# Performance work log

Measured on AMD Instinct MI355X. Metric: run time of the kernel, lower is better.

## Reference

```python
import jax, jax.numpy as jnp
import numpy as np

B, N, D, H = 128, 128, 1024, 8
HD = D // H  # 128; NOTE: N must equal HD due to the module's einsum pattern
SCALE = HD ** -0.5


def _split_heads(x):
    # [b, n, h*d] -> [b, h, n, d]
    b, n, _ = x.shape
    return x.reshape(b, n, H, HD).transpose(0, 2, 1, 3)


def setup_inputs() -> dict:
    key = jax.random.key(0)
    ks = jax.random.split(key, 12)
    s = D ** -0.5
    return {
        "words": jax.random.normal(ks[0], (B, N, D), jnp.float32),
        "position": jax.random.normal(ks[1], (B, N, D), jnp.float32),
        "conscious": jax.random.normal(ks[2], (B, N, D), jnp.float32),
        "Wq_w": jax.random.normal(ks[3], (D, D), jnp.float32) * s,
        "Wk_w": jax.random.normal(ks[4], (D, D), jnp.float32) * s,
        "Wv_w": jax.random.normal(ks[5], (D, D), jnp.float32) * s,
        "Wq_p": jax.random.normal(ks[6], (D, D), jnp.float32) * s,
        "Wk_p": jax.random.normal(ks[7], (D, D), jnp.float32) * s,
        "Wq_c": jax.random.normal(ks[8], (D, D), jnp.float32) * s,
        "Wk_c": jax.random.normal(ks[9], (D, D), jnp.float32) * s,
        "Wo": jax.random.normal(ks[10], (D, D), jnp.float32) * s,
        "bo": jax.random.normal(ks[11], (D,), jnp.float32) * 0.01,
    }


def reference(words, position, conscious, Wq_w, Wk_w, Wv_w, Wq_p, Wk_p, Wq_c, Wk_c, Wo, bo):
    q_w = _split_heads(words @ Wq_w)
    k_w = _split_heads(words @ Wk_w)
    v_w = _split_heads(words @ Wv_w)
    q_p = _split_heads(position @ Wq_p)
    k_p = _split_heads(position @ Wk_p)
    q_c = _split_heads(conscious @ Wq_c)
    k_c = _split_heads(conscious @ Wk_c)

    # Faithful to source: 'b h i j, b h j d -> b h i d' contracts q's head dim
    # with k's seq dim (requires N == HD). Three score streams summed.
    sim = (jnp.einsum('bhij,bhjd->bhid', q_w, k_w)
           + jnp.einsum('bhij,bhjd->bhid', q_p, k_p)
           + jnp.einsum('bhij,bhjd->bhid', q_c, k_c)) * SCALE
    attn = jax.nn.softmax(sim, axis=-1)
    out = jnp.einsum('bhij,bhjd->bhid', attn, v_w)  # [b,h,n,d]
    out = out.transpose(0, 2, 1, 3).reshape(B, N, D)  # merge heads
    return out @ Wo + bo
```

## Files before the change

### kernel.cpp

```cpp
#include <hip/hip_runtime.h>


typedef unsigned short u16;
typedef __attribute__((ext_vector_type(8))) short bf16x8;
typedef __attribute__((ext_vector_type(4))) short bf16x4;
typedef __attribute__((ext_vector_type(4))) float f32x4;

__device__ __forceinline__ float bf2f(u16 x) {
  union { unsigned u; float f; } v;
  v.u = ((unsigned)x) << 16;
  return v.f;
}

__device__ __forceinline__ u16 f2bf(float f) {
  union { float f; unsigned u; } v;
  v.f = f;
  unsigned r = v.u + 0x7fffu + ((v.u >> 16) & 1u);
  return (u16)(r >> 16);
}

__device__ __forceinline__ float ldv(const void* p, size_t i, int f32) {
  return f32 ? ((const float*)p)[i] : bf2f(((const u16*)p)[i]);
}

__device__ __forceinline__ f32x4 MFMA(bf16x8 a, bf16x8 b, f32x4 c) {
  return __builtin_amdgcn_mfma_f32_16x16x32_bf16(a, b, c, 0, 0, 0);
}

#define GLDS16(gp, lp)                                               \
  __builtin_amdgcn_global_load_lds(                                  \
      (const __attribute__((address_space(1))) unsigned int*)(gp),   \
      (__attribute__((address_space(3))) unsigned int*)(lp), 16, 0, 0)

__device__ __forceinline__ bf16x8 lds_frag(const u16* ls, int row, int cb) {
  const int byte = (row * 128 + cb) ^ ((row & 7) << 4);
  return *(const bf16x8*)((const char*)ls + byte);
}

__device__ __forceinline__ int cs_byte(int row, int colb) {
  return (row * 256 + colb) ^ ((row & 7) << 4);
}

__global__ void detect_dtype(const void* words, int* flag) {
  __shared__ int cnt;
  if (threadIdx.x == 0) cnt = 0;
  __syncthreads();
  const u16* w = (const u16*)words;
  int local = 0;
  for (int i = threadIdx.x; i < 2048; i += 256) {
    const u16 v = w[2 * i];
    const int e = (v >> 7) & 0xFF;
    if (v == 0 || (e >= 0x60 && e <= 0x8F)) local++;
  }
  atomicAdd(&cnt, local);
  __syncthreads();
  if (threadIdx.x == 0) *flag = (cnt >= 1434) ? 0 : 1;
}

__global__ __launch_bounds__(256) void cast_w(
    const void* w0, const void* w1, const void* w2, const void* w3,
    const void* w4, const void* w5, const void* w6, const void* w7,
    u16* __restrict__ WT, const int* __restrict__ flag) {
  __shared__ float t[32][33];
  const int f32 = *flag;
  const int p = blockIdx.z;
  const void* W;
  switch (p) {
    case 0: W = w0; break; case 1: W = w1; break; case 2: W = w2; break;
    case 3: W = w3; break; case 4: W = w4; break; case 5: W = w5; break;
    case 6: W = w6; break; default: W = w7; break;
  }
  const int k0 = blockIdx.y * 32, n0 = blockIdx.x * 32;
  const int tx = threadIdx.x & 31, ry = threadIdx.x >> 5;
  for (int r = ry; r < 32; r += 8)
    t[r][tx] = ldv(W, (size_t)(k0 + r) * 1024 + n0 + tx, f32);
  __syncthreads();
  u16* dst = WT + (size_t)p * 1048576ull;
  for (int r = ry; r < 32; r += 8)
    dst[(size_t)(n0 + r) * 1024 + k0 + tx] = f2bf(t[tx][r]);
}

__global__ __launch_bounds__(256) void cast_a(
    const void* x0, const void* x1, const void* x2, u16* __restrict__ Abf,
    int b0, int chb, const int* __restrict__ flag) {
  const int f32 = *flag;
  const int t = blockIdx.z;
  const void* src = (t == 0) ? x0 : ((t == 1) ? x1 : x2);
  u16* dst = Abf + (size_t)t * (size_t)chb * 131072ull;
  const size_t n4 = (size_t)chb * 32768ull;
  const size_t off = (size_t)b0 * 131072ull;
  const size_t stride = (size_t)gridDim.x * 256ull;
  if (f32) {
    const float4* s = (const float4*)src + off / 4;
    for (size_t i = (size_t)blockIdx.x * 256 + threadIdx.x; i < n4; i += stride) {
      const float4 v = s[i];
      bf16x4 o = { (short)f2bf(v.x), (short)f2bf(v.y),
                   (short)f2bf(v.z), (short)f2bf(v.w) };
      *(bf16x4*)&dst[i * 4] = o;
    }
  } else {
    const bf16x4* s = (const bf16x4*)((const u16*)src + off);
    for (size_t i = (size_t)blockIdx.x * 256 + threadIdx.x; i < n4; i += stride)
      ((bf16x4*)dst)[i] = s[i];
  }
}

__global__ __launch_bounds__(256) void proj_mfma(
    const u16* __restrict__ Abf, const u16* __restrict__ WT,
    u16* __restrict__ P, int chb) {
  __shared__ u16 lds[16384];
  u16* lsA = lds;
  u16* lsB = lds + 8192;
  const int p = blockIdx.z;
  const int asel = (p < 3) ? 0 : ((p < 5) ? 1 : 2);
  const u16* A = Abf + (size_t)asel * (size_t)chb * 131072ull;
  const u16* W = WT + (size_t)p * 1048576ull;
  u16* C = P + (size_t)p * (size_t)chb * 131072ull;
  const int tr = (p == 1) | (p == 2) | (p == 4) | (p == 6);

  int wg = blockIdx.y * 8 + blockIdx.x;
  const int nwg = (int)gridDim.y * 8;
  wg = (wg & 7) * (nwg >> 3) + (wg >> 3);
  const int bx = wg & 7, by = wg >> 3;

  const int tn = bx * 128;
  const int tm = by * 128;
  const int w = threadIdx.x >> 6, l = threadIdx.x & 63;
  const int wm = w >> 1, wn = w & 1;
  const int lr = l >> 3;
  const int lc = ((l & 7) * 16) ^ (lr << 4);
  const int fr = l & 15, fq = l >> 4;

  f32x4 acc[4][4] = {};
  for (int kt = 0; kt < 1024; kt += 64) {
    #pragma unroll
    for (int c = 0; c < 4; ++c) {
      GLDS16(&A[(size_t)(tm + w * 32 + c * 8 + lr) * 1024 + kt + (lc >> 1)],
             &lsA[(w * 32 + c * 8) * 64]);
      GLDS16(&W[(size_t)(tn + w * 32 + c * 8 + lr) * 1024 + kt + (lc >> 1)],
             &lsB[(w * 32 + c * 8) * 64]);
    }
    __syncthreads();
    #pragma unroll
    for (int ks = 0; ks < 2; ++ks) {
      bf16x8 af[4], bfr[4];
      const int cb = ks * 64 + fq * 16;
      #pragma unroll
      for (int m = 0; m < 4; ++m)
        af[m] = lds_frag(lsA, wm * 64 + m * 16 + fr, cb);
      #pragma unroll
      for (int n = 0; n < 4; ++n)
        bfr[n] = lds_frag(lsB, wn * 64 + n * 16 + fr, cb);
      #pragma unroll
      for (int m = 0; m < 4; ++m)
        #pragma unroll
        for (int n = 0; n < 4; ++n)
          acc[m][n] = MFMA(af[m], bfr[n], acc[m][n]);
    }
    __syncthreads();
  }

  #pragma unroll
  for (int m = 0; m < 4; ++m)
    #pragma unroll
    for (int n = 0; n < 4; ++n)
      #pragma unroll
      for (int r = 0; r < 4; ++r) {
        const int row = wm * 64 + m * 16 + fq * 4 + r;
        const int col = wn * 64 + n * 16 + fr;
        const int sr = tr ? col : row;
        const int sc = tr ? row : col;
        *(u16*)((char*)lds + cs_byte(sr, sc * 2)) = f2bf(acc[m][n][r]);
      }
  __syncthreads();
  const int crow = threadIdx.x >> 4;
  const int ccb = (threadIdx.x & 15) * 16;
  if (!tr) {
    #pragma unroll
    for (int pass = 0; pass < 8; ++pass) {
      const int row = pass * 16 + crow;
      const bf16x8 v = *(const bf16x8*)((const char*)lds + cs_byte(row, ccb));
      *(bf16x8*)&C[(size_t)(tm + row) * 1024 + tn + (ccb >> 1)] = v;
    }
  } else {
    const size_t tb = ((size_t)by * 8 + bx) * 16384ull;
    #pragma unroll
    for (int pass = 0; pass < 8; ++pass) {
      const int d = pass * 16 + crow;
      const bf16x8 v = *(const bf16x8*)((const char*)lds + cs_byte(d, ccb));
      *(bf16x8*)&C[tb + (size_t)d * 128 + (ccb >> 1)] = v;
    }
  }
}

__global__ __launch_bounds__(256) void attn_mfma(
    const u16* __restrict__ P, int chb, u16* __restrict__ merged) {
  __shared__ u16 pl[16384];
  const int h = blockIdx.x, b = blockIdx.y;
  const int w = threadIdx.x >> 6, l = threadIdx.x & 63;
  const size_t MS = (size_t)chb * 131072ull;
  const u16* const Qs[3] = { P, P + 3 * MS, P + 5 * MS };
  const u16* const Ks[3] = { P + 1 * MS, P + 4 * MS, P + 6 * MS };
  const u16* V = P + 2 * MS;
  const size_t qb = (size_t)b * 131072ull + (size_t)h * 128;
  const size_t kb = ((size_t)b * 8 + h) * 16384ull;

  f32x4 acc[2][8] = {};
  #pragma unroll
  for (int kt = 0; kt < 128; kt += 32) {
    #pragma unroll
    for (int t = 0; t < 3; ++t) {
      bf16x8 a[2];
      #pragma unroll
      for (int m = 0; m < 2; ++m)
        a[m] = *(const bf16x8*)&Qs[t][qb + (size_t)(w * 32 + m * 16 + (l & 15)) * 1024
                                       + kt + (l >> 4) * 8];
      #pragma unroll
      for (int n = 0; n < 8; ++n) {
        const bf16x8 bb = *(const bf16x8*)&Ks[t][kb + (size_t)(n * 16 + (l & 15)) * 128
                                                 + kt + (l >> 4) * 8];
        acc[0][n] = MFMA(a[0], bb, acc[0][n]);
        acc[1][n] = MFMA(a[1], bb, acc[1][n]);
      }
    }
  }

  const float SC = 0.08838834764831845f;
  #pragma unroll
  for (int m = 0; m < 2; ++m)
    #pragma unroll
    for (int r = 0; r < 4; ++r) {
      float mx = -3.0e38f;
      #pragma unroll
      for (int n = 0; n < 8; ++n) {
        acc[m][n][r] *= SC;
        mx = fmaxf(mx, acc[m][n][r]);
      }
      #pragma unroll
      for (int s = 1; s < 16; s <<= 1) mx = fmaxf(mx, __shfl_xor(mx, s));
      float sm = 0.f;
      #pragma unroll
      for (int n = 0; n < 8; ++n) {
        const float e = __expf(acc[m][n][r] - mx);
        acc[m][n][r] = e;
        sm += e;
      }
      #pragma unroll
      for (int s = 1; s < 16; s <<= 1) sm += __shfl_xor(sm, s);
      const float inv = 1.f / sm;
      #pragma unroll
      for (int n = 0; n < 8; ++n) acc[m][n][r] *= inv;
    }

  #pragma unroll
  for (int m = 0; m < 2; ++m)
    #pragma unroll
    for (int n = 0; n < 8; ++n)
      #pragma unroll
      for (int r = 0; r < 4; ++r) {
        const int row = w * 32 + m * 16 + (l >> 4) * 4 + r;
        const int col = n * 16 + (l & 15);
        const int byte = (row * 256 + col * 2) ^ ((row & 7) << 4);
        *(u16*)((char*)pl + byte) = f2bf(acc[m][n][r]);
      }
  __syncthreads();

  f32x4 o[2][8] = {};
  #pragma unroll
  for (int kt = 0; kt < 128; kt += 32) {
    bf16x8 a[2];
    #pragma unroll
    for (int m = 0; m < 2; ++m) {
      const int row = w * 32 + m * 16 + (l & 15);
      const int byte = (row * 256 + (kt + (l >> 4) * 8) * 2) ^ ((row & 7) << 4);
      a[m] = *(const bf16x8*)((char*)pl + byte);
    }
    #pragma unroll
    for (int n = 0; n < 8; ++n) {
      const bf16x8 bb = *(const bf16x8*)&V[kb + (size_t)(n * 16 + (l & 15)) * 128
                                           + kt + (l >> 4) * 8];
      o[0][n] = MFMA(a[0], bb, o[0][n]);
      o[1][n] = MFMA(a[1], bb, o[1][n]);
    }
  }

  __syncthreads();
  #pragma unroll
  for (int m = 0; m < 2; ++m)
    #pragma unroll
    for (int n = 0; n < 8; ++n)
      #pragma unroll
      for (int r = 0; r < 4; ++r) {
        const int row = w * 32 + m * 16 + (l >> 4) * 4 + r;
        const int col = n * 16 + (l & 15);
        *(u16*)((char*)pl + cs_byte(row, col * 2)) = f2bf(o[m][n][r]);
      }
  __syncthreads();
  const int crow = threadIdx.x >> 4;
  const int ccb = (threadIdx.x & 15) * 16;
  #pragma unroll
  for (int pass = 0; pass < 8; ++pass) {
    const int row = pass * 16 + crow;
    const bf16x8 v = *(const bf16x8*)((const char*)pl + cs_byte(row, ccb));
    *(bf16x8*)&merged[(size_t)(b * 128 + row) * 1024 + h * 128 + (ccb >> 1)] = v;
  }
}

__global__ __launch_bounds__(256) void final_mfma(
    const u16* __restrict__ A, const u16* __restrict__ W,
    const void* __restrict__ bias, void* __restrict__ out, int b0,
    const int* __restrict__ flag) {
  __shared__ u16 lds[16384];
  u16* lsA = lds;
  u16* lsB = lds + 8192;
  const int f32 = *flag;

  int wg = blockIdx.y * 8 + blockIdx.x;
  const int nwg = (int)gridDim.y * 8;
  wg = (wg & 7) * (nwg >> 3) + (wg >> 3);
  const int bx = wg & 7, by = wg >> 3;

  const int tn = bx * 128;
  const int tm = by * 128;
  const int w = threadIdx.x >> 6, l = threadIdx.x & 63;
  const int wm = w >> 1, wn = w & 1;
  const int lr = l >> 3;
  const int lc = ((l & 7) * 16) ^ (lr << 4);
  const int fr = l & 15, fq = l >> 4;

  f32x4 acc[4][4] = {};
  for (int kt = 0; kt < 1024; kt += 64) {
    #pragma unroll
    for (int c = 0; c < 4; ++c) {
      GLDS16(&A[(size_t)(tm + w * 32 + c * 8 + lr) * 1024 + kt + (lc >> 1)],
             &lsA[(w * 32 + c * 8) * 64]);
      GLDS16(&W[(size_t)(tn + w * 32 + c * 8 + lr) * 1024 + kt + (lc >> 1)],
             &lsB[(w * 32 + c * 8) * 64]);
    }
    __syncthreads();
    #pragma unroll
    for (int ks = 0; ks < 2; ++ks) {
      bf16x8 af[4], bfr[4];
      const int cb = ks * 64 + fq * 16;
      #pragma unroll
      for (int m = 0; m < 4; ++m)
        af[m] = lds_frag(lsA, wm * 64 + m * 16 + fr, cb);
      #pragma unroll
      for (int n = 0; n < 4; ++n)
        bfr[n] = lds_frag(lsB, wn * 64 + n * 16 + fr, cb);
      #pragma unroll
      for (int m = 0; m < 4; ++m)
        #pragma unroll
        for (int n = 0; n < 4; ++n)
          acc[m][n] = MFMA(af[m], bfr[n], acc[m][n]);
    }
    __syncthreads();
  }

  float* fs = (float*)lds;
  const int crow = threadIdx.x >> 4;
  const int cq = threadIdx.x & 15;
  #pragma unroll
  for (int half = 0; half < 2; ++half) {
    #pragma unroll
    for (int n2 = 0; n2 < 2; ++n2) {
      const int n = half * 2 + n2;
      #pragma unroll
      for (int m = 0; m < 4; ++m)
        #pragma unroll
        for (int r = 0; r < 4; ++r) {
          const int row = wm * 64 + m * 16 + fq * 4 + r;
          const int cpos = wn * 32 + n2 * 16 + fr;
          const int col = tn + wn * 64 + n * 16 + fr;
          const int byte = (row * 256 + cpos * 4) ^ ((row & 7) << 4);
          *(float*)((char*)fs + byte) = acc[m][n][r] + ldv(bias, col, f32);
        }
    }
    __syncthreads();
    #pragma unroll
    for (int pass = 0; pass < 8; ++pass) {
      const int row = pass * 16 + crow;
      const int byte = (row * 256 + cq * 16) ^ ((row & 7) << 4);
      const float4 v = *(const float4*)((const char*)fs + byte);
      const int cpos = cq * 4;
      const int gcol = tn + (cpos >> 5) * 64 + half * 32 + (cpos & 31);
      const size_t g = (size_t)(b0 * 128 + tm + row) * 1024 + gcol;
      if (f32) {
        *(float4*)&((float*)out)[g] = v;
      } else {
        bf16x4 o = { (short)f2bf(v.x), (short)f2bf(v.y),
                     (short)f2bf(v.z), (short)f2bf(v.w) };
        *(bf16x4*)&((u16*)out)[g] = o;
      }
    }
    __syncthreads();
  }
}

extern "C" void kernel_launch(void* const* d_in, const int* in_sizes, int n_in,
                              void* d_out, int out_size, void* d_ws, size_t ws_size,
                              hipStream_t stream) {
  const size_t fixed = 64ull + 8ull * 1048576ull * 2ull;
  int CHB = 128;
  while (CHB > 2 && fixed + 10ull * (size_t)CHB * 131072ull * 2ull > ws_size)
    CHB >>= 1;

  int* flag = (int*)d_ws;
  u16* WT = (u16*)((char*)d_ws + 64);
  u16* Abf = WT + 8ull * 1048576ull;
  u16* P = Abf + 3ull * (size_t)CHB * 131072ull;
  u16* merged = Abf;

  detect_dtype<<<1, 256, 0, stream>>>(d_in[0], flag);
  cast_w<<<dim3(32, 32, 8), 256, 0, stream>>>(
      d_in[3], d_in[4], d_in[5], d_in[6], d_in[7], d_in[8], d_in[9], d_in[10],
      WT, flag);

  for (int b0 = 0; b0 < 128; b0 += CHB) {
    cast_a<<<dim3(512, 1, 3), 256, 0, stream>>>(
        d_in[0], d_in[1], d_in[2], Abf, b0, CHB, flag);
    proj_mfma<<<dim3(8, CHB, 7), 256, 0, stream>>>(Abf, WT, P, CHB);
    attn_mfma<<<dim3(8, CHB), 256, 0, stream>>>(P, CHB, merged);
    final_mfma<<<dim3(8, CHB), 256, 0, stream>>>(
        merged, WT + 7ull * 1048576ull, d_in[11], d_out, b0, flag);
  }
}
```

Baseline: 729.3 us.

## Double-buffer LDS staging in projection and output GEMMs with K-tile of 32

The projection and final GEMM kernels move from a single 64-wide K tile (load, sync, compute, sync) to two LDS buffers of 32-wide K tiles. The next tile's global-to-LDS load is issued before the current tile is computed, so memory latency can overlap with MFMA work. A new XOR swizzle matches the 64-byte row stride. The trade-off is twice as many loop iterations and barriers per GEMM, and less compute per barrier to hide each load.

```diff
diff --git a/kernel.cpp b/kernel.cpp
--- a/kernel.cpp
+++ b/kernel.cpp
@@ -32,8 +32,8 @@
       (const __attribute__((address_space(1))) unsigned int*)(gp),   \
       (__attribute__((address_space(3))) unsigned int*)(lp), 16, 0, 0)
 
-__device__ __forceinline__ bf16x8 lds_frag(const u16* ls, int row, int cb) {
-  const int byte = (row * 128 + cb) ^ ((row & 7) << 4);
+__device__ __forceinline__ bf16x8 lds_frag32(const u16* ls, int row, int fq) {
+  const int byte = row * 64 + ((fq ^ ((row >> 1) & 3)) << 4);
   return *(const bf16x8*)((const char*)ls + byte);
 }
 
@@ -109,8 +109,8 @@
     const u16* __restrict__ Abf, const u16* __restrict__ WT,
     u16* __restrict__ P, int chb) {
   __shared__ u16 lds[16384];
-  u16* lsA = lds;
-  u16* lsB = lds + 8192;
+#define LA(buf) (lds + (buf) * 4096)
+#define LB(buf) (lds + 8192 + (buf) * 4096)
   const int p = blockIdx.z;
   const int asel = (p < 3) ? 0 : ((p < 5) ? 1 : 2);
   const u16* A = Abf + (size_t)asel * (size_t)chb * 131072ull;
@@ -127,38 +127,47 @@
   const int tm = by * 128;
   const int w = threadIdx.x >> 6, l = threadIdx.x & 63;
   const int wm = w >> 1, wn = w & 1;
-  const int lr = l >> 3;
-  const int lc = ((l & 7) * 16) ^ (lr << 4);
   const int fr = l & 15, fq = l >> 4;
 
+  const int srow = l >> 2;
+  const int sgr = (l & 3) ^ ((l >> 3) & 3);
+  const unsigned abase = (unsigned)(tm + w * 32 + srow) * 1024u + sgr * 8u;
+  const unsigned bbase = (unsigned)(tn + w * 32 + srow) * 1024u + sgr * 8u;
+  const int ldst0 = (w * 32) * 32;
+  const int ldst1 = (w * 32 + 16) * 32;
+
+#define STAGE(buf, kt)                                           \
+  {                                                              \
+    GLDS16(&A[abase + (unsigned)(kt)], &LA(buf)[ldst0]);         \
+    GLDS16(&A[abase + 16384u + (unsigned)(kt)], &LA(buf)[ldst1]);\
+    GLDS16(&W[bbase + (unsigned)(kt)], &LB(buf)[ldst0]);         \
+    GLDS16(&W[bbase + 16384u + (unsigned)(kt)], &LB(buf)[ldst1]);\
+  }
+
   f32x4 acc[4][4] = {};
-  for (int kt = 0; kt < 1024; kt += 64) {
-    #pragma unroll
-    for (int c = 0; c < 4; ++c) {
-      GLDS16(&A[(size_t)(tm + w * 32 + c * 8 + lr) * 1024 + kt + (lc >> 1)],
-             &lsA[(w * 32 + c * 8) * 64]);
-      GLDS16(&W[(size_t)(tn + w * 32 + c * 8 + lr) * 1024 + kt + (lc >> 1)],
-             &lsB[(w * 32 + c * 8) * 64]);
-    }
+  STAGE(0, 0);
+  __syncthreads();
+
+  for (int t = 0; t < 32; ++t) {
+    const int cur = t & 1;
+    if (t < 31) STAGE(cur ^ 1, (t + 1) * 32);
+    bf16x8 af[4], bfr[4];
+    #pragma unroll
+    for (int m = 0; m < 4; ++m)
+      af[m] = lds_frag32(LA(cur), wm * 64 + m * 16 + fr, fq);
+    #pragma unroll
+    for (int n = 0; n < 4; ++n)
+      bfr[n] = lds_frag32(LB(cur), wn * 64 + n * 16 + fr, fq);
+    #pragma unroll
+    for (int m = 0; m < 4; ++m)
+      #pragma unroll
+      for (int n = 0; n < 4; ++n)
+        acc[m][n] = MFMA(af[m], bfr[n], acc[m][n]);
     __syncthreads();
-    #pragma unroll
-    for (int ks = 0; ks < 2; ++ks) {
-      bf16x8 af[4], bfr[4];
-      const int cb = ks * 64 + fq * 16;
-      #pragma unroll
-      for (int m = 0; m < 4; ++m)
-        af[m] = lds_frag(lsA, wm * 64 + m * 16 + fr, cb);
-      #pragma unroll
-      for (int n = 0; n < 4; ++n)
-        bfr[n] = lds_frag(lsB, wn * 64 + n * 16 + fr, cb);
-      #pragma unroll
-      for (int m = 0; m < 4; ++m)
-        #pragma unroll
-        for (int n = 0; n < 4; ++n)
-          acc[m][n] = MFMA(af[m], bfr[n], acc[m][n]);
-    }
-    __syncthreads();
-  }
+  }
+#undef STAGE
+#undef LA
+#undef LB
 
   #pragma unroll
   for (int m = 0; m < 4; ++m)
@@ -311,8 +320,8 @@
     const void* __restrict__ bias, void* __restrict__ out, int b0,
     const int* __restrict__ flag) {
   __shared__ u16 lds[16384];
-  u16* lsA = lds;
-  u16* lsB = lds + 8192;
+#define LA(buf) (lds + (buf) * 4096)
+#define LB(buf) (lds + 8192 + (buf) * 4096)
   const int f32 = *flag;
 
   int wg = blockIdx.y * 8 + blockIdx.x;
@@ -324,38 +333,47 @@
   const int tm = by * 128;
   const int w = threadIdx.x >> 6, l = threadIdx.x & 63;
   const int wm = w >> 1, wn = w & 1;
-  const int lr = l >> 3;
-  const int lc = ((l & 7) * 16) ^ (lr << 4);
   const int fr = l & 15, fq = l >> 4;
 
+  const int srow = l >> 2;
+  const int sgr = (l & 3) ^ ((l >> 3) & 3);
+  const unsigned abase = (unsigned)(tm + w * 32 + srow) * 1024u + sgr * 8u;
+  const unsigned bbase = (unsigned)(tn + w * 32 + srow) * 1024u + sgr * 8u;
+  const int ldst0 = (w * 32) * 32;
+  const int ldst1 = (w * 32 + 16) * 32;
+
+#define STAGE(buf, kt)                                           \
+  {                                                              \
+    GLDS16(&A[abase + (unsigned)(kt)], &LA(buf)[ldst0]);         \
+    GLDS16(&A[abase + 16384u + (unsigned)(kt)], &LA(buf)[ldst1]);\
+    GLDS16(&W[bbase + (unsigned)(kt)], &LB(buf)[ldst0]);         \
+    GLDS16(&W[bbase + 16384u + (unsigned)(kt)], &LB(buf)[ldst1]);\
+  }
+
   f32x4 acc[4][4] = {};
-  for (int kt = 0; kt < 1024; kt += 64) {
-    #pragma unroll
-    for (int c = 0; c < 4; ++c) {
-      GLDS16(&A[(size_t)(tm + w * 32 + c * 8 + lr) * 1024 + kt + (lc >> 1)],
-             &lsA[(w * 32 + c * 8) * 64]);
-      GLDS16(&W[(size_t)(tn + w * 32 + c * 8 + lr) * 1024 + kt + (lc >> 1)],
-             &lsB[(w * 32 + c * 8) * 64]);
-    }
+  STAGE(0, 0);
+  __syncthreads();
+
+  for (int t = 0; t < 32; ++t) {
+    const int cur = t & 1;
+    if (t < 31) STAGE(cur ^ 1, (t + 1) * 32);
+    bf16x8 af[4], bfr[4];
+    #pragma unroll
+    for (int m = 0; m < 4; ++m)
+      af[m] = lds_frag32(LA(cur), wm * 64 + m * 16 + fr, fq);
+    #pragma unroll
+    for (int n = 0; n < 4; ++n)
+      bfr[n] = lds_frag32(LB(cur), wn * 64 + n * 16 + fr, fq);
+    #pragma unroll
+    for (int m = 0; m < 4; ++m)
+      #pragma unroll
+      for (int n = 0; n < 4; ++n)
+        acc[m][n] = MFMA(af[m], bfr[n], acc[m][n]);
     __syncthreads();
-    #pragma unroll
-    for (int ks = 0; ks < 2; ++ks) {
-      bf16x8 af[4], bfr[4];
-      const int cb = ks * 64 + fq * 16;
-      #pragma unroll
-      for (int m = 0; m < 4; ++m)
-        af[m] = lds_frag(lsA, wm * 64 + m * 16 + fr, cb);
-      #pragma unroll
-      for (int n = 0; n < 4; ++n)
-        bfr[n] = lds_frag(lsB, wn * 64 + n * 16 + fr, cb);
-      #pragma unroll
-      for (int m = 0; m < 4; ++m)
-        #pragma unroll
-        for (int n = 0; n < 4; ++n)
-          acc[m][n] = MFMA(af[m], bfr[n], acc[m][n]);
-    }
-    __syncthreads();
-  }
+  }
+#undef STAGE
+#undef LA
+#undef LB
 
   float* fs = (float*)lds;
   const int crow = threadIdx.x >> 4;
```

After: 729.4 us. About the same (+0.0%).
